# Kernel tuning notes

Measured on AMD Instinct MI355X. Metric: run time of the kernel, lower is better.

## Reference

```python
import jax, jax.numpy as jnp
from jax import lax
import numpy as np

B, INP, WIDTH, OUTP, E, H = 32, 1024, 256, 1024, 8, 14
EPS = 1e-5


def setup_inputs() -> dict:
    key = jax.random.key(0)
    ks = jax.random.split(key, 12)
    n = lambda k, s, sc=0.05: jax.random.normal(k, s, jnp.float32) * sc
    return {
        "x": jax.random.normal(ks[0], (B, INP, H, H), jnp.float32),
        "w1": n(ks[1], (E, WIDTH, INP, 1, 1)),
        "w2": n(ks[2], (E, WIDTH, WIDTH, 3, 3)),
        "w3": n(ks[3], (E, OUTP, WIDTH, 1, 1)),
        "r1_w": n(ks[4], (INP, E)), "r1_b": jnp.zeros((E,), jnp.float32),
        "r2_w": n(ks[5], (WIDTH, E)), "r2_b": jnp.zeros((E,), jnp.float32),
        "r3_w": n(ks[6], (WIDTH, E)), "r3_b": jnp.zeros((E,), jnp.float32),
        "bn1_g": jax.random.uniform(ks[7], (WIDTH,), jnp.float32, 0.5, 1.5),
        "bn1_b": n(ks[8], (WIDTH,), 0.1),
        "bn1_m": jnp.zeros((WIDTH,), jnp.float32), "bn1_v": jnp.ones((WIDTH,), jnp.float32),
        "bn2_g": jax.random.uniform(ks[9], (WIDTH,), jnp.float32, 0.5, 1.5),
        "bn2_b": n(ks[10], (WIDTH,), 0.1),
        "bn2_m": jnp.zeros((WIDTH,), jnp.float32), "bn2_v": jnp.ones((WIDTH,), jnp.float32),
        "bn3_g": jax.random.uniform(ks[11], (OUTP,), jnp.float32, 0.5, 1.5),
        "bn3_b": jnp.zeros((OUTP,), jnp.float32),
        "bn3_m": jnp.zeros((OUTP,), jnp.float32), "bn3_v": jnp.ones((OUTP,), jnp.float32),
    }


def _route(x, w, b):
    # global avg pool -> linear -> sigmoid : [B, E]
    return jax.nn.sigmoid(x.mean(axis=(2, 3)) @ w + b)


def _cond_conv(x, w, rw, stride=1, padding=0, dilation=1, groups=1):
    # x: [B,Cin,H,W]; w: [E,Cout,Cin/groups,kh,kw]; rw: [B,E]
    Bn, Cin, Hh, Ww = x.shape
    _, Cout, Cin_g, kh, kw = w.shape
    # per-sample expert-combined kernels, then batch-grouped conv
    cw = jnp.einsum('be,eoikl->boikl', rw, w).reshape(Bn * Cout, Cin_g, kh, kw)
    out = lax.conv_general_dilated(
        x.reshape(1, Bn * Cin, Hh, Ww), cw,
        window_strides=(stride, stride),
        padding=[(padding, padding), (padding, padding)],
        rhs_dilation=(dilation, dilation),
        feature_group_count=Bn * groups,
        dimension_numbers=('NCHW', 'OIHW', 'NCHW'))
    return out.reshape(Bn, Cout, out.shape[2], out.shape[3])


def _bn(x, g, b, m, v):
    inv = lax.rsqrt(v + EPS) * g
    return x * inv[None, :, None, None] + (b - m * inv)[None, :, None, None]


def reference(x, w1, w2, w3, r1_w, r1_b, r2_w, r2_b, r3_w, r3_b,
              bn1_g, bn1_b, bn1_m, bn1_v, bn2_g, bn2_b, bn2_m, bn2_v,
              bn3_g, bn3_b, bn3_m, bn3_v):
    identity = x
    rw1 = _route(x, r1_w, r1_b)
    out = jax.nn.relu(_bn(_cond_conv(x, w1, rw1), bn1_g, bn1_b, bn1_m, bn1_v))
    rw2 = _route(out, r2_w, r2_b)
    out = jax.nn.relu(_bn(_cond_conv(out, w2, rw2, stride=1, padding=1), bn2_g, bn2_b, bn2_m, bn2_v))
    rw3 = _route(out, r3_w, r3_b)
    out = _bn(_cond_conv(out, w3, rw3), bn3_g, bn3_b, bn3_m, bn3_v)
    return jax.nn.relu(out + identity)
```

## Files before the change

### kernel.cpp

```cpp
#include <hip/hip_runtime.h>
#include <hip/hip_bf16.h>

#define BB 32
#define INP 1024
#define WIDTH 256
#define OUTP 1024
#define NE 8
#define HW 196
#define HH 14
#define EPS 1e-5f

#define S1 (WIDTH * INP)
#define S2 (WIDTH * WIDTH * 9)
#define S3 (OUTP * WIDTH)

typedef __attribute__((ext_vector_type(8))) short bf16x8;
typedef __attribute__((ext_vector_type(4))) float f32x4;
typedef __attribute__((ext_vector_type(8))) unsigned short u16x8;


#define VMCNT(n) asm volatile("s_waitcnt vmcnt(" #n ")" ::: "memory")

__device__ __forceinline__ unsigned short f2bf_bits(float f) {
    unsigned u = __float_as_uint(f);
    u += 0x7FFFu + ((u >> 16) & 1u);
    return (unsigned short)(u >> 16);
}
__device__ __forceinline__ float bf2f(unsigned short h) {
    return __uint_as_float((unsigned)h << 16);
}

#if defined(__has_builtin)
#if __has_builtin(__builtin_amdgcn_global_load_lds)
#define HAVE_GLL 1
#endif
#endif
__device__ __forceinline__ void gl2lds(const unsigned short* g, unsigned short* l,
                                       int lane) {
#ifdef HAVE_GLL
    __builtin_amdgcn_global_load_lds(
        (const __attribute__((address_space(1))) unsigned int*)(const void*)g,
        (__attribute__((address_space(3))) unsigned int*)(void*)l, 16, 0, 0);
#else
    *(u16x8*)(l + lane * 8) = *(const u16x8*)g;
#endif
}

__device__ __forceinline__ void block_route(
    const float* __restrict__ vec, const float* __restrict__ W,
    const float* __restrict__ bias, float scale, int C, int g,
    float* srw, int tid) {
    int wv = tid >> 6, lane = tid & 63;
    float p0[NE], p1[NE];
#pragma unroll
    for (int e = 0; e < NE; e++) { p0[e] = 0.f; p1[e] = 0.f; }
    const float* v0 = vec + (size_t)(g * 8 + wv * 2) * C;
    const float* v1 = v0 + C;
    for (int c = lane; c < C; c += 64) {
        float4 wa = *(const float4*)(W + c * 8);
        float4 wb = *(const float4*)(W + c * 8 + 4);
        float m0 = v0[c], m1 = v1[c];
        p0[0] += m0 * wa.x; p0[1] += m0 * wa.y; p0[2] += m0 * wa.z; p0[3] += m0 * wa.w;
        p0[4] += m0 * wb.x; p0[5] += m0 * wb.y; p0[6] += m0 * wb.z; p0[7] += m0 * wb.w;
        p1[0] += m1 * wa.x; p1[1] += m1 * wa.y; p1[2] += m1 * wa.z; p1[3] += m1 * wa.w;
        p1[4] += m1 * wb.x; p1[5] += m1 * wb.y; p1[6] += m1 * wb.z; p1[7] += m1 * wb.w;
    }
#pragma unroll
    for (int j = 1; j < 64; j <<= 1) {
#pragma unroll
        for (int e = 0; e < NE; e++) {
            p0[e] += __shfl_xor(p0[e], j, 64);
            p1[e] += __shfl_xor(p1[e], j, 64);
        }
    }
    if (lane == 0) {
#pragma unroll
        for (int e = 0; e < NE; e++) {
            srw[(wv * 2) * 8 + e] = 1.0f / (1.0f + expf(-(scale * p0[e] + bias[e])));
            srw[(wv * 2 + 1) * 8 + e] = 1.0f / (1.0f + expf(-(scale * p1[e] + bias[e])));
        }
    }
    __syncthreads();
}

__global__ __launch_bounds__(256) void pre_kernel(
    const float* __restrict__ x, unsigned short* __restrict__ xb,
    float* __restrict__ mean1,
    const float* __restrict__ w2, unsigned short* __restrict__ wb2,
    unsigned short* __restrict__ zpad,
    float* __restrict__ msum2, float* __restrict__ msum3) {
    __shared__ __align__(16) char smem[128 * 17 * 4];
    int blk = blockIdx.x, t = threadIdx.x;
    if (blk < 256) {
        float (*lt)[17] = (float(*)[17])smem;
        int b = blk >> 3, yq = blk & 7, c0 = yq * 128;
        int cr = t >> 1, half = t & 1;
        const float* src = x + ((size_t)(b * INP + c0 + cr)) * HW;
        float msum = 0.f;
        int j = t >> 4, nl = t & 15;
        for (int pg = 0; pg < 14; pg++) {
            int p0 = pg * 16 + half * 8;
            float vv[8];
            if (pg < 12) {
                float4 a = *(const float4*)(src + p0);
                float4 c = *(const float4*)(src + p0 + 4);
                vv[0] = a.x; vv[1] = a.y; vv[2] = a.z; vv[3] = a.w;
                vv[4] = c.x; vv[5] = c.y; vv[6] = c.z; vv[7] = c.w;
            } else {
#pragma unroll
                for (int i = 0; i < 8; i++) {
                    int p = p0 + i;
                    vv[i] = (p < HW) ? src[p] : 0.f;
                }
            }
#pragma unroll
            for (int i = 0; i < 8; i++) { msum += vv[i]; lt[cr][half * 8 + i] = vv[i]; }
            __syncthreads();
            unsigned short pk[8];
#pragma unroll
            for (int i = 0; i < 8; i++) pk[i] = f2bf_bits(lt[j * 8 + i][nl]);
            size_t tile = ((size_t)b * 14 + pg) * 32 + (size_t)(yq * 4 + (j >> 2));
            int lane = nl | ((j & 3) << 4);
            *(u16x8*)(xb + tile * 512 + lane * 8) = *(u16x8*)pk;
            __syncthreads();
        }
        float other = __shfl_xor(msum, 1, 64);
        if (half == 0) mean1[b * INP + c0 + cr] = (msum + other) * (1.0f / (float)HW);
    } else {
        unsigned short* lds = (unsigned short*)smem;
        int eo = blk - 256;
        if (eo < 32) {
            int idx = eo * 256 + t;
            msum2[idx] = 0.f;
            msum3[idx] = 0.f;
            if (eo == 0 && t == 0) {
                u16x8 z = {0, 0, 0, 0, 0, 0, 0, 0};
                *(u16x8*)zpad = z;
            }
        }
        const float* src = w2 + (size_t)eo * 2304 + (size_t)t * 9;
#pragma unroll
        for (int t9 = 0; t9 < 9; t9++) lds[t9 * 256 + t] = f2bf_bits(src[t9]);
        __syncthreads();
        unsigned short* dst = wb2 + (size_t)eo * 2304;
        for (int j = t; j < 288; j += 256)
            *(u16x8*)(dst + j * 8) = *(const u16x8*)(lds + j * 8);
    }
}

__global__ __launch_bounds__(256) void combine_cont_r(
    const float* __restrict__ w, const float* __restrict__ vec,
    const float* __restrict__ rW, const float* __restrict__ rB, float scale, int C,
    unsigned short* __restrict__ cw, int S, int Mt, int Kt) {
    __shared__ float srw[64];
    int tid = threadIdx.x, wv = tid >> 6, lane = tid & 63, ml = lane & 15, k8l = lane >> 4;
    int g = blockIdx.y;
    block_route(vec, rW, rB, scale, C, g, srw, tid);
    int kq = Kt >> 2;
    int mt = blockIdx.x / kq, kt = (blockIdx.x - mt * kq) * 4 + wv;
    int K = Kt * 32;
    const float* src = w + (size_t)(mt * 16 + ml) * K + kt * 32 + k8l * 8;
    float v[NE][8];
#pragma unroll
    for (int e = 0; e < NE; e++) {
        float4 a = *(const float4*)(src + (size_t)e * S);
        float4 c = *(const float4*)(src + (size_t)e * S + 4);
        v[e][0] = a.x; v[e][1] = a.y; v[e][2] = a.z; v[e][3] = a.w;
        v[e][4] = c.x; v[e][5] = c.y; v[e][6] = c.z; v[e][7] = c.w;
    }
    size_t dto = ((size_t)mt * Kt + kt) * 512 + (size_t)lane * 8;
    size_t bstr = (size_t)Mt * Kt * 512;
    for (int bl = 0; bl < 8; bl++) {
        int b = g * 8 + bl;
        float acc[8];
#pragma unroll
        for (int jj = 0; jj < 8; jj++) acc[jj] = 0.f;
#pragma unroll
        for (int e = 0; e < NE; e++) {
            float r = srw[bl * NE + e];
#pragma unroll
            for (int jj = 0; jj < 8; jj++) acc[jj] += r * v[e][jj];
        }
        u16x8 o;
#pragma unroll
        for (int jj = 0; jj < 8; jj++) o[jj] = f2bf_bits(acc[jj]);
        *(u16x8*)(cw + (size_t)b * bstr + dto) = o;
    }
}

__global__ __launch_bounds__(256) void combine_w2_r(
    const unsigned short* __restrict__ wb2, const float* __restrict__ vec,
    const float* __restrict__ rW, const float* __restrict__ rB, float scale,
    unsigned short* __restrict__ cw) {
    __shared__ float srw[64];
    int tid = threadIdx.x, wv = tid >> 6, lane = tid & 63, ol = lane & 15, g4 = lane >> 4;
    int g = blockIdx.y;
    block_route(vec, rW, rB, scale, 256, g, srw, tid);
    int ot = blockIdx.x / 18, kt = (blockIdx.x - ot * 18) * 4 + wv;
    const unsigned short* src = wb2 + (size_t)(ot * 16 + ol) * 2304 + kt * 32 + g4 * 8;
    float v[NE][8];
#pragma unroll
    for (int e = 0; e < NE; e++) {
        u16x8 raw = *(const u16x8*)(src + (size_t)e * S2);
#pragma unroll
        for (int jj = 0; jj < 8; jj++) v[e][jj] = bf2f(raw[jj]);
    }
    size_t dto = ((size_t)ot * 72 + kt) * 512 + (size_t)lane * 8;
    for (int bl = 0; bl < 8; bl++) {
        int b = g * 8 + bl;
        float acc[8];
#pragma unroll
        for (int jj = 0; jj < 8; jj++) acc[jj] = 0.f;
#pragma unroll
        for (int e = 0; e < NE; e++) {
            float r = srw[bl * NE + e];
#pragma unroll
            for (int jj = 0; jj < 8; jj++) acc[jj] += r * v[e][jj];
        }
        u16x8 out;
#pragma unroll
        for (int jj = 0; jj < 8; jj++) out[jj] = f2bf_bits(acc[jj]);
        *(u16x8*)(cw + (size_t)b * (16 * 72 * 512) + dto) = out;
    }
}

__device__ __forceinline__ void epilogue_act(
    const f32x4* acc, int b, int mt, int nt0, int nB, int lo, int g4,
    const float* __restrict__ g, const float* __restrict__ be,
    const float* __restrict__ mu, const float* __restrict__ var,
    unsigned short* __restrict__ actout, float* __restrict__ msum) {
    int c0 = mt * 16 + g4 * 4;
    float sc[4], sh[4];
#pragma unroll
    for (int r = 0; r < 4; r++) {
        float iv = rsqrtf(var[c0 + r] + EPS) * g[c0 + r];
        sc[r] = iv;
        sh[r] = be[c0 + r] - mu[c0 + r] * iv;
    }
    float ms[4] = {0.f, 0.f, 0.f, 0.f};
    int ktc = mt >> 1;
    int lanehi = ((mt * 2 + (g4 >> 1)) & 3) << 4;
#pragma unroll
    for (int t = 0; t < 4; t++) {
        if (t >= nB) break;
        int nt = nt0 + t;
        int n = nt * 16 + lo;
        float v[4];
#pragma unroll
        for (int r = 0; r < 4; r++) {
            float val = acc[t][r] * sc[r] + sh[r];
            val = fmaxf(val, 0.f);
            if (n >= HW) val = 0.f;
            v[r] = val;
            ms[r] += val;
        }
        unsigned p01 = (unsigned)f2bf_bits(v[0]) | ((unsigned)f2bf_bits(v[1]) << 16);
        unsigned p23 = (unsigned)f2bf_bits(v[2]) | ((unsigned)f2bf_bits(v[3]) << 16);
        size_t off = (((size_t)(b * 14 + nt)) * 8 + ktc) * 512 + (size_t)(lo | lanehi) * 8 + (g4 & 1) * 4;
        *(uint2*)(actout + off) = make_uint2(p01, p23);
    }
#pragma unroll
    for (int r = 0; r < 4; r++) {
        float s = ms[r];
        s += __shfl_xor(s, 1, 64);
        s += __shfl_xor(s, 2, 64);
        s += __shfl_xor(s, 4, 64);
        s += __shfl_xor(s, 8, 64);
        if (lo == 0) atomicAdd(&msum[b * 256 + c0 + r], s);
    }
}

__global__ __launch_bounds__(512) void gemm1_fused(
    const unsigned short* __restrict__ Bsw, const unsigned short* __restrict__ Asw,
    const float* __restrict__ g, const float* __restrict__ be,
    const float* __restrict__ mu, const float* __restrict__ var,
    unsigned short* __restrict__ actout, float* __restrict__ msum) {
    __shared__ __align__(16) unsigned short lAb[8][4 * 512];
    __shared__ __align__(16) unsigned short lBb[8][4 * 512];
    const int Kt = 32;
    int b = blockIdx.x, mh = blockIdx.y, z = blockIdx.z;
    int nt0 = (z < 3) ? z * 4 : 11;
    int nB = (z < 2) ? 4 : 3;
    int tid = threadIdx.x, wv = tid >> 6, grp = wv >> 2, wl = wv & 3;
    int lane = tid & 63, lo = lane & 15, g4 = lane >> 4;
    const unsigned short* Ab = Asw + (size_t)(b * 16 + mh * 4) * Kt * 512;
    const unsigned short* Bb = Bsw + (size_t)(b * 14 + nt0) * Kt * 512;
    f32x4 acc[4];
#pragma unroll
    for (int t = 0; t < 4; t++) acc[t] = {0.f, 0.f, 0.f, 0.f};

    auto stage = [&](int kt) {
        unsigned short* lA = lAb[kt & 7];
        unsigned short* lB = lBb[kt & 7];
        gl2lds(Ab + ((size_t)wl * Kt + kt) * 512 + lane * 8, lA + wl * 512, lane);
        if (wl < nB)
            gl2lds(Bb + ((size_t)wl * Kt + kt) * 512 + lane * 8, lB + wl * 512, lane);
    };
    auto compute = [&](int kt) {
        const unsigned short* lA = lAb[kt & 7];
        const unsigned short* lB = lBb[kt & 7];
        bf16x8 a0 = *(const bf16x8*)(lA + wl * 512 + lane * 8);
#pragma unroll
        for (int t = 0; t < 4; t++) {
            if (t >= nB) break;
            bf16x8 bt = *(const bf16x8*)(lB + t * 512 + lane * 8);
            acc[t] = __builtin_amdgcn_mfma_f32_16x16x32_bf16(a0, bt, acc[t], 0, 0, 0);
        }
    };

    stage(grp);
    stage(grp + 2);
    for (int kp = 0; kp < 16; kp++) {
        int c = 2 * kp + grp;
        if (c + 2 < 32) {
            if (wl < nB) VMCNT(2); else VMCNT(1);
        } else {
            VMCNT(0);
        }
        __builtin_amdgcn_s_barrier();
        int s = c + 4;
        if (s < 32) stage(s);
        compute(c);
    }
    __syncthreads();
    float* red = (float*)&lBb[0][0];
    if (grp == 1) {
#pragma unroll
        for (int t = 0; t < 4; t++)
            *(f32x4*)(red + (((size_t)wl * 4 + t) * 64 + lane) * 4) = acc[t];
    }
    __syncthreads();
    if (grp == 0) {
#pragma unroll
        for (int t = 0; t < 4; t++) {
            f32x4 o = *(const f32x4*)(red + (((size_t)wl * 4 + t) * 64 + lane) * 4);
#pragma unroll
            for (int r = 0; r < 4; r++) acc[t][r] += o[r];
        }
        epilogue_act(acc, b, mh * 4 + wl, nt0, nB, lo, g4, g, be, mu, var, actout, msum);
    }
}

__global__ __launch_bounds__(512) void gemm2_fused(
    const unsigned short* __restrict__ act, const unsigned short* __restrict__ cw2,
    const unsigned short* __restrict__ zpad,
    const float* __restrict__ g, const float* __restrict__ be,
    const float* __restrict__ mu, const float* __restrict__ var,
    unsigned short* __restrict__ actout, float* __restrict__ msum) {
    __shared__ __align__(16) unsigned short lAb[8][4 * 512];
    __shared__ __align__(16) unsigned short lBb[8][4 * 512];
    int b = blockIdx.x, mh = blockIdx.y, z = blockIdx.z;
    int nt0 = (z < 3) ? z * 4 : 11;
    int nB = (z < 2) ? 4 : 3;
    int tid = threadIdx.x, wv = tid >> 6, grp = wv >> 2, wl = wv & 3;
    int lane = tid & 63, lo = lane & 15, g4 = lane >> 4;
    const unsigned short* Ab = cw2 + (size_t)(b * 16 + mh * 4) * 72 * 512;
    const unsigned short* actb = act + (size_t)b * 14 * 8 * 512;

    int p0 = (nt0 + wl) * 16 + lo;
    int py0 = p0 / HH, px0 = p0 - (p0 / HH) * HH;
    bool pv0 = (wl < nB) && (p0 < HW);

    f32x4 acc[4];
#pragma unroll
    for (int t = 0; t < 4; t++) acc[t] = {0.f, 0.f, 0.f, 0.f};

    auto stage = [&](int kt) {
        unsigned short* lA = lAb[kt & 7];
        unsigned short* lB = lBb[kt & 7];
        gl2lds(Ab + ((size_t)wl * 72 + kt) * 512 + lane * 8, lA + wl * 512, lane);
        if (wl < nB) {
            int t9 = kt >> 3;
            int dy = t9 / 3 - 1, dx = t9 - (t9 / 3) * 3 - 1;
            int itile = kt & 7;
            int sy = py0 + dy, sx = px0 + dx;
            bool ok = pv0 && sy >= 0 && sy < HH && sx >= 0 && sx < HH;
            int ns = sy * HH + sx;
            const unsigned short* gp = ok
                ? actb + ((size_t)(ns >> 4) * 8 + itile) * 512 + (size_t)((ns & 15) | (g4 << 4)) * 8
                : zpad;
            gl2lds(gp, lB + wl * 512, lane);
        }
    };
    auto compute = [&](int kt) {
        const unsigned short* lA = lAb[kt & 7];
        const unsigned short* lB = lBb[kt & 7];
        bf16x8 a0 = *(const bf16x8*)(lA + wl * 512 + lane * 8);
#pragma unroll
        for (int t = 0; t < 4; t++) {
            if (t >= nB) break;
            bf16x8 bt = *(const bf16x8*)(lB + t * 512 + lane * 8);
            acc[t] = __builtin_amdgcn_mfma_f32_16x16x32_bf16(a0, bt, acc[t], 0, 0, 0);
        }
    };

    stage(grp);
    stage(grp + 2);
    for (int kp = 0; kp < 36; kp++) {
        int c = 2 * kp + grp;
        if (c + 2 < 72) {
            if (wl < nB) VMCNT(2); else VMCNT(1);
        } else {
            VMCNT(0);
        }
        __builtin_amdgcn_s_barrier();
        int s = c + 4;
        if (s < 72) stage(s);
        compute(c);
    }
    __syncthreads();
    float* red = (float*)&lBb[0][0];
    if (grp == 1) {
#pragma unroll
        for (int t = 0; t < 4; t++)
            *(f32x4*)(red + (((size_t)wl * 4 + t) * 64 + lane) * 4) = acc[t];
    }
    __syncthreads();
    if (grp == 0) {
#pragma unroll
        for (int t = 0; t < 4; t++) {
            f32x4 o = *(const f32x4*)(red + (((size_t)wl * 4 + t) * 64 + lane) * 4);
#pragma unroll
            for (int r = 0; r < 4; r++) acc[t][r] += o[r];
        }
        epilogue_act(acc, b, mh * 4 + wl, nt0, nB, lo, g4, g, be, mu, var, actout, msum);
    }
}

__global__ __launch_bounds__(512) void gemm3_fused(
    const unsigned short* __restrict__ Bsw, const unsigned short* __restrict__ Asw,
    const float* __restrict__ g, const float* __restrict__ be,
    const float* __restrict__ mu, const float* __restrict__ var,
    const unsigned short* __restrict__ xb, float* __restrict__ out) {
    __shared__ __align__(16) unsigned short lAb[4][8 * 512];
    __shared__ __align__(16) unsigned short lBb[4][7 * 512];
    int b = blockIdx.x, y = blockIdx.y, mh = y >> 1, nh = y & 1;
    int tid = threadIdx.x, wv = tid >> 6, grp = wv >> 2, wl = wv & 3;
    int lane = tid & 63, lo = lane & 15, g4 = lane >> 4;
    const unsigned short* Ab = Asw + (size_t)(b * 64 + mh * 8) * 8 * 512;
    const unsigned short* Bb = Bsw + (size_t)(b * 14 + nh * 7) * 8 * 512;
    f32x4 acc0[7], acc1[7];
#pragma unroll
    for (int t = 0; t < 7; t++) { acc0[t] = {0.f, 0.f, 0.f, 0.f}; acc1[t] = {0.f, 0.f, 0.f, 0.f}; }

    auto stage = [&](int kt, unsigned short* lA, unsigned short* lB) {
        gl2lds(Ab + ((size_t)wl * 8 + kt) * 512 + lane * 8, lA + wl * 512, lane);
        gl2lds(Ab + ((size_t)(wl + 4) * 8 + kt) * 512 + lane * 8, lA + (wl + 4) * 512, lane);
        gl2lds(Bb + ((size_t)wl * 8 + kt) * 512 + lane * 8, lB + wl * 512, lane);
        if (wl < 3)
            gl2lds(Bb + ((size_t)(4 + wl) * 8 + kt) * 512 + lane * 8, lB + (4 + wl) * 512, lane);
    };
    auto compute = [&](const unsigned short* lA, const unsigned short* lB) {
        bf16x8 a0 = *(const bf16x8*)(lA + wl * 512 + lane * 8);
        bf16x8 a1 = *(const bf16x8*)(lA + (wl + 4) * 512 + lane * 8);
#pragma unroll
        for (int t = 0; t < 7; t++) {
            bf16x8 bt = *(const bf16x8*)(lB + t * 512 + lane * 8);
            acc0[t] = __builtin_amdgcn_mfma_f32_16x16x32_bf16(a0, bt, acc0[t], 0, 0, 0);
            acc1[t] = __builtin_amdgcn_mfma_f32_16x16x32_bf16(a1, bt, acc1[t], 0, 0, 0);
        }
    };

    stage(grp, lAb[grp], lBb[grp]);
    for (int kp = 0; kp < 4; kp++) {
        __syncthreads();
        if (kp < 3) {
            int s = 2 * kp + 2 + grp;
            stage(s, lAb[s & 3], lBb[s & 3]);
        }
        int c = (2 * kp + grp) & 3;
        compute(lAb[c], lBb[c]);
    }
    __syncthreads();
    float* red = (float*)&lBb[0][0];
    if (grp == 1) {
#pragma unroll
        for (int t = 0; t < 7; t++)
            *(f32x4*)(red + (((size_t)wl * 7 + t) * 64 + lane) * 4) = acc0[t];
    }
    __syncthreads();
    if (grp == 0) {
#pragma unroll
        for (int t = 0; t < 7; t++) {
            f32x4 o = *(const f32x4*)(red + (((size_t)wl * 7 + t) * 64 + lane) * 4);
#pragma unroll
            for (int r = 0; r < 4; r++) acc0[t][r] += o[r];
        }
    }
    __syncthreads();
    if (grp == 1) {
#pragma unroll
        for (int t = 0; t < 7; t++)
            *(f32x4*)(red + (((size_t)wl * 7 + t) * 64 + lane) * 4) = acc1[t];
    }
    __syncthreads();
    if (grp != 0) return;
#pragma unroll
    for (int t = 0; t < 7; t++) {
        f32x4 o = *(const f32x4*)(red + (((size_t)wl * 7 + t) * 64 + lane) * 4);
#pragma unroll
        for (int r = 0; r < 4; r++) acc1[t][r] += o[r];
    }

#pragma unroll
    for (int a = 0; a < 2; a++) {
        int mt = mh * 8 + wl + 4 * a;
        int c0 = mt * 16 + g4 * 4;
        float sc[4], sh[4];
#pragma unroll
        for (int r = 0; r < 4; r++) {
            float iv = rsqrtf(var[c0 + r] + EPS) * g[c0 + r];
            sc[r] = iv;
            sh[r] = be[c0 + r] - mu[c0 + r] * iv;
        }
        int ktc = mt >> 1;
        int lanehi = ((mt * 2 + (g4 >> 1)) & 3) << 4;
#pragma unroll
        for (int t = 0; t < 7; t++) {
            int nt = nh * 7 + t;
            int n = nt * 16 + lo;
            if (n >= HW) continue;
            const unsigned short* xr = xb + (((size_t)(b * 14 + nt)) * 32 + ktc) * 512
                                       + (size_t)(lo | lanehi) * 8 + (g4 & 1) * 4;
            uint2 rv = *(const uint2*)xr;
            float res[4] = {bf2f((unsigned short)(rv.x & 0xffff)),
                            bf2f((unsigned short)(rv.x >> 16)),
                            bf2f((unsigned short)(rv.y & 0xffff)),
                            bf2f((unsigned short)(rv.y >> 16))};
            f32x4 av = a ? acc1[t] : acc0[t];
#pragma unroll
            for (int r = 0; r < 4; r++) {
                size_t oidx = ((size_t)(b * OUTP + c0 + r)) * HW + n;
                float val = av[r] * sc[r] + sh[r] + res[r];
                out[oidx] = fmaxf(val, 0.f);
            }
        }
    }
}

extern "C" void kernel_launch(void* const* d_in, const int* in_sizes, int n_in,
                              void* d_out, int out_size, void* d_ws, size_t ws_size,
                              hipStream_t stream) {
    const float* x    = (const float*)d_in[0];
    const float* w1   = (const float*)d_in[1];
    const float* w2   = (const float*)d_in[2];
    const float* w3   = (const float*)d_in[3];
    const float* r1_w = (const float*)d_in[4];
    const float* r1_b = (const float*)d_in[5];
    const float* r2_w = (const float*)d_in[6];
    const float* r2_b = (const float*)d_in[7];
    const float* r3_w = (const float*)d_in[8];
    const float* r3_b = (const float*)d_in[9];
    const float* bn1_g = (const float*)d_in[10];
    const float* bn1_b = (const float*)d_in[11];
    const float* bn1_m = (const float*)d_in[12];
    const float* bn1_v = (const float*)d_in[13];
    const float* bn2_g = (const float*)d_in[14];
    const float* bn2_b = (const float*)d_in[15];
    const float* bn2_m = (const float*)d_in[16];
    const float* bn2_v = (const float*)d_in[17];
    const float* bn3_g = (const float*)d_in[18];
    const float* bn3_b = (const float*)d_in[19];
    const float* bn3_m = (const float*)d_in[20];
    const float* bn3_v = (const float*)d_in[21];
    float* out = (float*)d_out;

    char* ws = (char*)d_ws;
    size_t off = 0;
    float* mean1 = (float*)(ws + off); off += (size_t)BB * INP * 4;
    float* msum2 = (float*)(ws + off); off += (size_t)BB * 256 * 4;
    float* msum3 = (float*)(ws + off); off += (size_t)BB * 256 * 4;
    unsigned short* zpad = (unsigned short*)(ws + off); off += 256;
    off = (off + 255) & ~(size_t)255;
    unsigned short* act1 = (unsigned short*)(ws + off); off += (size_t)BB * 14 * 8 * 512 * 2;
    unsigned short* act2 = (unsigned short*)(ws + off); off += (size_t)BB * 14 * 8 * 512 * 2;
    unsigned short* cw2 = (unsigned short*)(ws + off); off += (size_t)BB * 16 * 72 * 512 * 2;
    unsigned short* xb  = (unsigned short*)(ws + off); off += (size_t)BB * 14 * 32 * 512 * 2;
    unsigned short* wb2 = (unsigned short*)(ws + off); off += (size_t)S2 * NE * 2;
    unsigned short* cwX = (unsigned short*)(ws + off); off += (size_t)BB * S1 * 2;
    unsigned short* cw1 = cwX;
    unsigned short* cw3 = cwX;
    (void)ws_size;

    pre_kernel<<<2304, 256, 0, stream>>>(x, xb, mean1, w2, wb2, zpad, msum2, msum3);

    combine_cont_r<<<dim3(128, 4), 256, 0, stream>>>(w1, mean1, r1_w, r1_b, 1.0f, INP,
                                                     cw1, S1, 16, 32);
    gemm1_fused<<<dim3(BB, 4, 4), 512, 0, stream>>>(xb, cw1, bn1_g, bn1_b, bn1_m, bn1_v,
                                                    act1, msum2);

    combine_w2_r<<<dim3(288, 4), 256, 0, stream>>>(wb2, msum2, r2_w, r2_b,
                                                   1.0f / (float)HW, cw2);
    gemm2_fused<<<dim3(BB, 4, 4), 512, 0, stream>>>(act1, cw2, zpad, bn2_g, bn2_b,
                                                    bn2_m, bn2_v, act2, msum3);

    combine_cont_r<<<dim3(128, 4), 256, 0, stream>>>(w3, msum3, r3_w, r3_b,
                                                     1.0f / (float)HW, WIDTH,
                                                     cw3, S3, 64, 8);
    gemm3_fused<<<dim3(BB, 16), 512, 0, stream>>>(act2, cw3, bn3_g, bn3_b, bn3_m, bn3_v,
                                                  xb, out);
}
```

Before: 243.3 us.

## Fuse all seven stages into one cooperative persistent kernel with grid syncs

Replaces the chain of seven kernel launches with a single cooperative mega-kernel of 512 blocks that runs each phase (pre-pack, combines, three GEMMs) separated by grid.sync barriers. This removes launch overhead and inter-kernel gaps. Phases that used more blocks (e.g. pre_kernel with 2304 blocks) are remapped onto 512 blocks. The old multi-kernel path remains as a fallback when the stream is being captured or occupancy is insufficient. The cost is grid-wide barriers, 64KB static LDS per block limiting occupancy, and phases with lower parallelism per block.

```diff
diff --git a/kernel.cpp b/kernel.cpp
--- a/kernel.cpp
+++ b/kernel.cpp
@@ -1,5 +1,8 @@
 #include <hip/hip_runtime.h>
 #include <hip/hip_bf16.h>
+#include <hip/hip_cooperative_groups.h>
+
+namespace cg = cooperative_groups;
 
 #define BB 32
 #define INP 1024
@@ -45,6 +48,7 @@
     *(u16x8*)(l + lane * 8) = *(const u16x8*)g;
 #endif
 }
+
 
 __device__ __forceinline__ void block_route(
     const float* __restrict__ vec, const float* __restrict__ W,
@@ -538,65 +542,566 @@
     }
 }
 
+
+struct MegaP {
+    const float *x, *w1, *w2, *w3;
+    const float *r1w, *r1b, *r2w, *r2b, *r3w, *r3b;
+    const float *bn1g, *bn1b, *bn1m, *bn1v;
+    const float *bn2g, *bn2b, *bn2m, *bn2v;
+    const float *bn3g, *bn3b, *bn3m, *bn3v;
+    float* out;
+    float *mean1, *msum2, *msum3;
+    unsigned short *zpad, *act1, *act2, *cw2, *xb, *wb2, *cwX;
+};
+
+__device__ __forceinline__ void route512(
+    const float* vec, const float* W, const float* bias, float scale, int C,
+    int g, float* srw, int tid) {
+    int wv = tid >> 6, lane = tid & 63;
+    float pp[NE];
+#pragma unroll
+    for (int e = 0; e < NE; e++) pp[e] = 0.f;
+    const float* v0 = vec + (size_t)(g * 8 + wv) * C;
+    for (int c = lane; c < C; c += 64) {
+        float4 wa = *(const float4*)(W + c * 8);
+        float4 wb = *(const float4*)(W + c * 8 + 4);
+        float m = v0[c];
+        pp[0] += m * wa.x; pp[1] += m * wa.y; pp[2] += m * wa.z; pp[3] += m * wa.w;
+        pp[4] += m * wb.x; pp[5] += m * wb.y; pp[6] += m * wb.z; pp[7] += m * wb.w;
+    }
+#pragma unroll
+    for (int j = 1; j < 64; j <<= 1) {
+#pragma unroll
+        for (int e = 0; e < NE; e++) pp[e] += __shfl_xor(pp[e], j, 64);
+    }
+    if (lane == 0) {
+#pragma unroll
+        for (int e = 0; e < NE; e++)
+            srw[wv * 8 + e] = 1.0f / (1.0f + expf(-(scale * pp[e] + bias[e])));
+    }
+    __syncthreads();
+}
+
+__device__ __forceinline__ void phase_pre(const MegaP& p, char* smem, int r, int tid) {
+    if (r < 256) {
+        float (*lt)[17] = (float(*)[17])smem;
+        bool act = tid < 256;
+        int b = r >> 3, yq = r & 7, c0 = yq * 128;
+        int cr = tid >> 1, half = tid & 1;
+        const float* src = act ? p.x + ((size_t)(b * INP + c0 + cr)) * HW : p.x;
+        float msum = 0.f;
+        int j = tid >> 4, nl = tid & 15;
+        for (int pg = 0; pg < 14; pg++) {
+            if (act) {
+                int p0 = pg * 16 + half * 8;
+                float vv[8];
+                if (pg < 12) {
+                    float4 a = *(const float4*)(src + p0);
+                    float4 c = *(const float4*)(src + p0 + 4);
+                    vv[0] = a.x; vv[1] = a.y; vv[2] = a.z; vv[3] = a.w;
+                    vv[4] = c.x; vv[5] = c.y; vv[6] = c.z; vv[7] = c.w;
+                } else {
+#pragma unroll
+                    for (int i = 0; i < 8; i++) {
+                        int pp = p0 + i;
+                        vv[i] = (pp < HW) ? src[pp] : 0.f;
+                    }
+                }
+#pragma unroll
+                for (int i = 0; i < 8; i++) { msum += vv[i]; lt[cr][half * 8 + i] = vv[i]; }
+            }
+            __syncthreads();
+            if (act) {
+                unsigned short pk[8];
+#pragma unroll
+                for (int i = 0; i < 8; i++) pk[i] = f2bf_bits(lt[j * 8 + i][nl]);
+                size_t tile = ((size_t)b * 14 + pg) * 32 + (size_t)(yq * 4 + (j >> 2));
+                int lane = nl | ((j & 3) << 4);
+                *(u16x8*)(p.xb + tile * 512 + lane * 8) = *(u16x8*)pk;
+            }
+            __syncthreads();
+        }
+        if (act) {
+            float other = __shfl_xor(msum, 1, 64);
+            if (half == 0) p.mean1[b * INP + c0 + cr] = (msum + other) * (1.0f / (float)HW);
+        }
+    } else {
+        int rb = r - 256;
+        int sub = tid >> 8, vt = tid & 255;
+        unsigned short* lds = (unsigned short*)smem + sub * 2304;
+        if (rb < 32 && tid < 256) {
+            int idx = rb * 256 + tid;
+            p.msum2[idx] = 0.f;
+            p.msum3[idx] = 0.f;
+        }
+        if (rb == 0 && tid == 0) {
+            u16x8 z = {0, 0, 0, 0, 0, 0, 0, 0};
+            *(u16x8*)p.zpad = z;
+        }
+        for (int it = 0; it < 4; it++) {
+            int eo = rb * 8 + it * 2 + sub;
+            const float* s2 = p.w2 + (size_t)eo * 2304 + (size_t)vt * 9;
+#pragma unroll
+            for (int t9 = 0; t9 < 9; t9++) lds[t9 * 256 + vt] = f2bf_bits(s2[t9]);
+            __syncthreads();
+            unsigned short* dst = p.wb2 + (size_t)eo * 2304;
+            for (int jj = vt; jj < 288; jj += 256)
+                *(u16x8*)(dst + jj * 8) = *(const u16x8*)(lds + jj * 8);
+            __syncthreads();
+        }
+    }
+}
+
+__device__ __forceinline__ void phase_combine_cont(
+    const float* w, const float* vec, const float* rW, const float* rB,
+    float scale, int C, unsigned short* cw, int S, int Mt, int Kt,
+    char* smem, int r, int tid) {
+    if (r >= 256) return;
+    float* srw = (float*)smem;
+    int wv = tid >> 6, lane = tid & 63, ml = lane & 15, k8l = lane >> 4;
+    int g = r & 3, xp = r >> 2;
+    route512(vec, rW, rB, scale, C, g, srw, tid);
+    int kq8 = Kt >> 3;
+    int mt = xp / kq8, kt = (xp - mt * kq8) * 8 + wv;
+    int K = Kt * 32;
+    const float* src = w + (size_t)(mt * 16 + ml) * K + kt * 32 + k8l * 8;
+    float v[NE][8];
+#pragma unroll
+    for (int e = 0; e < NE; e++) {
+        float4 a = *(const float4*)(src + (size_t)e * S);
+        float4 c = *(const float4*)(src + (size_t)e * S + 4);
+        v[e][0] = a.x; v[e][1] = a.y; v[e][2] = a.z; v[e][3] = a.w;
+        v[e][4] = c.x; v[e][5] = c.y; v[e][6] = c.z; v[e][7] = c.w;
+    }
+    size_t dto = ((size_t)mt * Kt + kt) * 512 + (size_t)lane * 8;
+    size_t bstr = (size_t)Mt * Kt * 512;
+    for (int bl = 0; bl < 8; bl++) {
+        int b = g * 8 + bl;
+        float acc[8];
+#pragma unroll
+        for (int jj = 0; jj < 8; jj++) acc[jj] = 0.f;
+#pragma unroll
+        for (int e = 0; e < NE; e++) {
+            float rr = srw[bl * NE + e];
+#pragma unroll
+            for (int jj = 0; jj < 8; jj++) acc[jj] += rr * v[e][jj];
+        }
+        u16x8 o;
+#pragma unroll
+        for (int jj = 0; jj < 8; jj++) o[jj] = f2bf_bits(acc[jj]);
+        *(u16x8*)(cw + (size_t)b * bstr + dto) = o;
+    }
+}
+
+__device__ __forceinline__ void phase_combine_w2(const MegaP& p, char* smem,
+                                                 int r, int tid) {
+    float* srw = (float*)smem;
+    int wv = tid >> 6, lane = tid & 63, ol = lane & 15, g4 = lane >> 4;
+    int g = r & 3, u = r >> 2;
+    route512(p.msum2, p.r2w, p.r2b, 1.0f / (float)HW, 256, g, srw, tid);
+    for (int it = 0; it < 2; it++) {
+        int bx;
+        if (it == 0) bx = u + (wv >= 4 ? 128 : 0);
+        else {
+            if (wv >= 4 || u >= 32) break;
+            bx = u + 256;
+        }
+        int ot = bx / 18, ktq = bx - ot * 18;
+        int kt = ktq * 4 + (wv & 3);
+        const unsigned short* src = p.wb2 + (size_t)(ot * 16 + ol) * 2304 + kt * 32 + g4 * 8;
+        float v[NE][8];
+#pragma unroll
+        for (int e = 0; e < NE; e++) {
+            u16x8 raw = *(const u16x8*)(src + (size_t)e * S2);
+#pragma unroll
+            for (int jj = 0; jj < 8; jj++) v[e][jj] = bf2f(raw[jj]);
+        }
+        size_t dto = ((size_t)ot * 72 + kt) * 512 + (size_t)lane * 8;
+        for (int bl = 0; bl < 8; bl++) {
+            int b = g * 8 + bl;
+            float acc[8];
+#pragma unroll
+            for (int jj = 0; jj < 8; jj++) acc[jj] = 0.f;
+#pragma unroll
+            for (int e = 0; e < NE; e++) {
+                float rr = srw[bl * NE + e];
+#pragma unroll
+                for (int jj = 0; jj < 8; jj++) acc[jj] += rr * v[e][jj];
+            }
+            u16x8 o;
+#pragma unroll
+            for (int jj = 0; jj < 8; jj++) o[jj] = f2bf_bits(acc[jj]);
+            *(u16x8*)(p.cw2 + (size_t)b * (16 * 72 * 512) + dto) = o;
+        }
+    }
+}
+
+__device__ __forceinline__ void phase_gemm1(const MegaP& p, char* smem, int r, int tid) {
+    unsigned short (*lAb)[4 * 512] = (unsigned short(*)[4 * 512])smem;
+    unsigned short (*lBb)[4 * 512] = (unsigned short(*)[4 * 512])(smem + 32768);
+    const int Kt = 32;
+    int b = r >> 4, mh = (r >> 2) & 3, z = r & 3;
+    int nt0 = (z < 3) ? z * 4 : 11;
+    int nB = (z < 2) ? 4 : 3;
+    int wv = tid >> 6, grp = wv >> 2, wl = wv & 3;
+    int lane = tid & 63, lo = lane & 15, g4 = lane >> 4;
+    const unsigned short* Ab = p.cwX + (size_t)(b * 16 + mh * 4) * Kt * 512;
+    const unsigned short* Bb = p.xb + (size_t)(b * 14 + nt0) * Kt * 512;
+    f32x4 acc[4];
+#pragma unroll
+    for (int t = 0; t < 4; t++) acc[t] = {0.f, 0.f, 0.f, 0.f};
+
+    auto stage = [&](int kt) {
+        unsigned short* lA = lAb[kt & 7];
+        unsigned short* lB = lBb[kt & 7];
+        gl2lds(Ab + ((size_t)wl * Kt + kt) * 512 + lane * 8, lA + wl * 512, lane);
+        if (wl < nB)
+            gl2lds(Bb + ((size_t)wl * Kt + kt) * 512 + lane * 8, lB + wl * 512, lane);
+    };
+    auto compute = [&](int kt) {
+        const unsigned short* lA = lAb[kt & 7];
+        const unsigned short* lB = lBb[kt & 7];
+        bf16x8 a0 = *(const bf16x8*)(lA + wl * 512 + lane * 8);
+#pragma unroll
+        for (int t = 0; t < 4; t++) {
+            if (t >= nB) break;
+            bf16x8 bt = *(const bf16x8*)(lB + t * 512 + lane * 8);
+            acc[t] = __builtin_amdgcn_mfma_f32_16x16x32_bf16(a0, bt, acc[t], 0, 0, 0);
+        }
+    };
+
+    stage(grp);
+    stage(grp + 2);
+    for (int kp = 0; kp < 16; kp++) {
+        int c = 2 * kp + grp;
+        if (c + 2 < 32) {
+            if (wl < nB) VMCNT(2); else VMCNT(1);
+        } else {
+            VMCNT(0);
+        }
+        __builtin_amdgcn_s_barrier();
+        int s = c + 4;
+        if (s < 32) stage(s);
+        compute(c);
+    }
+    __syncthreads();
+    float* red = (float*)&lBb[0][0];
+    if (grp == 1) {
+#pragma unroll
+        for (int t = 0; t < 4; t++)
+            *(f32x4*)(red + (((size_t)wl * 4 + t) * 64 + lane) * 4) = acc[t];
+    }
+    __syncthreads();
+    if (grp == 0) {
+#pragma unroll
+        for (int t = 0; t < 4; t++) {
+            f32x4 o = *(const f32x4*)(red + (((size_t)wl * 4 + t) * 64 + lane) * 4);
+#pragma unroll
+            for (int rr = 0; rr < 4; rr++) acc[t][rr] += o[rr];
+        }
+        epilogue_act(acc, b, mh * 4 + wl, nt0, nB, lo, g4,
+                     p.bn1g, p.bn1b, p.bn1m, p.bn1v, p.act1, p.msum2);
+    }
+}
+
+__device__ __forceinline__ void phase_gemm2(const MegaP& p, char* smem, int r, int tid) {
+    unsigned short (*lAb)[4 * 512] = (unsigned short(*)[4 * 512])smem;
+    unsigned short (*lBb)[4 * 512] = (unsigned short(*)[4 * 512])(smem + 32768);
+    int b = r >> 4, mh = (r >> 2) & 3, z = r & 3;
+    int nt0 = (z < 3) ? z * 4 : 11;
+    int nB = (z < 2) ? 4 : 3;
+    int wv = tid >> 6, grp = wv >> 2, wl = wv & 3;
+    int lane = tid & 63, lo = lane & 15, g4 = lane >> 4;
+    const unsigned short* Ab = p.cw2 + (size_t)(b * 16 + mh * 4) * 72 * 512;
+    const unsigned short* actb = p.act1 + (size_t)b * 14 * 8 * 512;
+
+    int p0 = (nt0 + wl) * 16 + lo;
+    int py0 = p0 / HH, px0 = p0 - (p0 / HH) * HH;
+    bool pv0 = (wl < nB) && (p0 < HW);
+
+    f32x4 acc[4];
+#pragma unroll
+    for (int t = 0; t < 4; t++) acc[t] = {0.f, 0.f, 0.f, 0.f};
+
+    auto stage = [&](int kt) {
+        unsigned short* lA = lAb[kt & 7];
+        unsigned short* lB = lBb[kt & 7];
+        gl2lds(Ab + ((size_t)wl * 72 + kt) * 512 + lane * 8, lA + wl * 512, lane);
+        if (wl < nB) {
+            int t9 = kt >> 3;
+            int dy = t9 / 3 - 1, dx = t9 - (t9 / 3) * 3 - 1;
+            int itile = kt & 7;
+            int sy = py0 + dy, sx = px0 + dx;
+            bool ok = pv0 && sy >= 0 && sy < HH && sx >= 0 && sx < HH;
+            int ns = sy * HH + sx;
+            const unsigned short* gp = ok
+                ? actb + ((size_t)(ns >> 4) * 8 + itile) * 512 + (size_t)((ns & 15) | (g4 << 4)) * 8
+                : p.zpad;
+            gl2lds(gp, lB + wl * 512, lane);
+        }
+    };
+    auto compute = [&](int kt) {
+        const unsigned short* lA = lAb[kt & 7];
+        const unsigned short* lB = lBb[kt & 7];
+        bf16x8 a0 = *(const bf16x8*)(lA + wl * 512 + lane * 8);
+#pragma unroll
+        for (int t = 0; t < 4; t++) {
+            if (t >= nB) break;
+            bf16x8 bt = *(const bf16x8*)(lB + t * 512 + lane * 8);
+            acc[t] = __builtin_amdgcn_mfma_f32_16x16x32_bf16(a0, bt, acc[t], 0, 0, 0);
+        }
+    };
+
+    stage(grp);
+    stage(grp + 2);
+    for (int kp = 0; kp < 36; kp++) {
+        int c = 2 * kp + grp;
+        if (c + 2 < 72) {
+            if (wl < nB) VMCNT(2); else VMCNT(1);
+        } else {
+            VMCNT(0);
+        }
+        __builtin_amdgcn_s_barrier();
+        int s = c + 4;
+        if (s < 72) stage(s);
+        compute(c);
+    }
+    __syncthreads();
+    float* red = (float*)&lBb[0][0];
+    if (grp == 1) {
+#pragma unroll
+        for (int t = 0; t < 4; t++)
+            *(f32x4*)(red + (((size_t)wl * 4 + t) * 64 + lane) * 4) = acc[t];
+    }
+    __syncthreads();
+    if (grp == 0) {
+#pragma unroll
+        for (int t = 0; t < 4; t++) {
+            f32x4 o = *(const f32x4*)(red + (((size_t)wl * 4 + t) * 64 + lane) * 4);
+#pragma unroll
+            for (int rr = 0; rr < 4; rr++) acc[t][rr] += o[rr];
+        }
+        epilogue_act(acc, b, mh * 4 + wl, nt0, nB, lo, g4,
+                     p.bn2g, p.bn2b, p.bn2m, p.bn2v, p.act2, p.msum3);
+    }
+}
+
+__device__ __forceinline__ void phase_gemm3(const MegaP& p, char* smem, int r, int tid) {
+    unsigned short (*lAb)[8 * 512] = (unsigned short(*)[8 * 512])smem;
+    unsigned short (*lBb)[7 * 512] = (unsigned short(*)[7 * 512])(smem + 32768);
+    int b = r >> 4, y = r & 15, mh = y >> 1, nh = y & 1;
+    int wv = tid >> 6, grp = wv >> 2, wl = wv & 3;
+    int lane = tid & 63, lo = lane & 15, g4 = lane >> 4;
+    const unsigned short* Ab = p.cwX + (size_t)(b * 64 + mh * 8) * 8 * 512;
+    const unsigned short* Bb = p.act2 + (size_t)(b * 14 + nh * 7) * 8 * 512;
+    f32x4 acc0[7], acc1[7];
+#pragma unroll
+    for (int t = 0; t < 7; t++) { acc0[t] = {0.f, 0.f, 0.f, 0.f}; acc1[t] = {0.f, 0.f, 0.f, 0.f}; }
+
+    auto stage = [&](int kt, unsigned short* lA, unsigned short* lB) {
+        gl2lds(Ab + ((size_t)wl * 8 + kt) * 512 + lane * 8, lA + wl * 512, lane);
+        gl2lds(Ab + ((size_t)(wl + 4) * 8 + kt) * 512 + lane * 8, lA + (wl + 4) * 512, lane);
+        gl2lds(Bb + ((size_t)wl * 8 + kt) * 512 + lane * 8, lB + wl * 512, lane);
+        if (wl < 3)
+            gl2lds(Bb + ((size_t)(4 + wl) * 8 + kt) * 512 + lane * 8, lB + (4 + wl) * 512, lane);
+    };
+    auto compute = [&](const unsigned short* lA, const unsigned short* lB) {
+        bf16x8 a0 = *(const bf16x8*)(lA + wl * 512 + lane * 8);
+        bf16x8 a1 = *(const bf16x8*)(lA + (wl + 4) * 512 + lane * 8);
+#pragma unroll
+        for (int t = 0; t < 7; t++) {
+            bf16x8 bt = *(const bf16x8*)(lB + t * 512 + lane * 8);
+            acc0[t] = __builtin_amdgcn_mfma_f32_16x16x32_bf16(a0, bt, acc0[t], 0, 0, 0);
+            acc1[t] = __builtin_amdgcn_mfma_f32_16x16x32_bf16(a1, bt, acc1[t], 0, 0, 0);
+        }
+    };
+
+    stage(grp, lAb[grp], lBb[grp]);
+    for (int kp = 0; kp < 4; kp++) {
+        __syncthreads();
+        if (kp < 3) {
+            int s = 2 * kp + 2 + grp;
+            stage(s, lAb[s & 3], lBb[s & 3]);
+        }
+        int c = (2 * kp + grp) & 3;
+        compute(lAb[c], lBb[c]);
+    }
+    __syncthreads();
+    float* red = (float*)&lBb[0][0];
+    if (grp == 1) {
+#pragma unroll
+        for (int t = 0; t < 7; t++)
+            *(f32x4*)(red + (((size_t)wl * 7 + t) * 64 + lane) * 4) = acc0[t];
+    }
+    __syncthreads();
+    if (grp == 0) {
+#pragma unroll
+        for (int t = 0; t < 7; t++) {
+            f32x4 o = *(const f32x4*)(red + (((size_t)wl * 7 + t) * 64 + lane) * 4);
+#pragma unroll
+            for (int rr = 0; rr < 4; rr++) acc0[t][rr] += o[rr];
+        }
+    }
+    __syncthreads();
+    if (grp == 1) {
+#pragma unroll
+        for (int t = 0; t < 7; t++)
+            *(f32x4*)(red + (((size_t)wl * 7 + t) * 64 + lane) * 4) = acc1[t];
+    }
+    __syncthreads();
+    if (grp != 0) return;
+#pragma unroll
+    for (int t = 0; t < 7; t++) {
+        f32x4 o = *(const f32x4*)(red + (((size_t)wl * 7 + t) * 64 + lane) * 4);
+#pragma unroll
+        for (int rr = 0; rr < 4; rr++) acc1[t][rr] += o[rr];
+    }
+
+#pragma unroll
+    for (int a = 0; a < 2; a++) {
+        int mt = mh * 8 + wl + 4 * a;
+        int c0 = mt * 16 + g4 * 4;
+        float sc[4], sh[4];
+#pragma unroll
+        for (int rr = 0; rr < 4; rr++) {
+            float iv = rsqrtf(p.bn3v[c0 + rr] + EPS) * p.bn3g[c0 + rr];
+            sc[rr] = iv;
+            sh[rr] = p.bn3b[c0 + rr] - p.bn3m[c0 + rr] * iv;
+        }
+        int ktc = mt >> 1;
+        int lanehi = ((mt * 2 + (g4 >> 1)) & 3) << 4;
+#pragma unroll
+        for (int t = 0; t < 7; t++) {
+            int nt = nh * 7 + t;
+            int n = nt * 16 + lo;
+            if (n >= HW) continue;
+            const unsigned short* xr = p.xb + (((size_t)(b * 14 + nt)) * 32 + ktc) * 512
+                                       + (size_t)(lo | lanehi) * 8 + (g4 & 1) * 4;
+            uint2 rv = *(const uint2*)xr;
+            float res[4] = {bf2f((unsigned short)(rv.x & 0xffff)),
+                            bf2f((unsigned short)(rv.x >> 16)),
+                            bf2f((unsigned short)(rv.y & 0xffff)),
+                            bf2f((unsigned short)(rv.y >> 16))};
+            f32x4 av = a ? acc1[t] : acc0[t];
+#pragma unroll
+            for (int rr = 0; rr < 4; rr++) {
+                size_t oidx = ((size_t)(b * OUTP + c0 + rr)) * HW + n;
+                float val = av[rr] * sc[rr] + sh[rr] + res[rr];
+                p.out[oidx] = fmaxf(val, 0.f);
+            }
+        }
+    }
+}
+
+__global__ __launch_bounds__(512, 4) void mega_kernel(MegaP p) {
+    __shared__ __align__(16) char smem[65536];
+    cg::grid_group grid = cg::this_grid();
+    const int r = blockIdx.x;
+    const int tid = threadIdx.x;
+
+    phase_pre(p, smem, r, tid);
+    __threadfence(); grid.sync(); __threadfence();
+
+    phase_combine_cont(p.w1, p.mean1, p.r1w, p.r1b, 1.0f, INP,
+                       p.cwX, S1, 16, 32, smem, r, tid);
+    __threadfence(); grid.sync(); __threadfence();
+
+    phase_gemm1(p, smem, r, tid);
+    __threadfence(); grid.sync(); __threadfence();
+
+    phase_combine_w2(p, smem, r, tid);
+    __threadfence(); grid.sync(); __threadfence();
+
+    phase_gemm2(p, smem, r, tid);
+    __threadfence(); grid.sync(); __threadfence();
+
+    phase_combine_cont(p.w3, p.msum3, p.r3w, p.r3b, 1.0f / (float)HW, WIDTH,
+                       p.cwX, S3, 64, 8, smem, r, tid);
+    __threadfence(); grid.sync(); __threadfence();
+
+    phase_gemm3(p, smem, r, tid);
+}
+
 extern "C" void kernel_launch(void* const* d_in, const int* in_sizes, int n_in,
                               void* d_out, int out_size, void* d_ws, size_t ws_size,
                               hipStream_t stream) {
-    const float* x    = (const float*)d_in[0];
-    const float* w1   = (const float*)d_in[1];
-    const float* w2   = (const float*)d_in[2];
-    const float* w3   = (const float*)d_in[3];
-    const float* r1_w = (const float*)d_in[4];
-    const float* r1_b = (const float*)d_in[5];
-    const float* r2_w = (const float*)d_in[6];
-    const float* r2_b = (const float*)d_in[7];
-    const float* r3_w = (const float*)d_in[8];
-    const float* r3_b = (const float*)d_in[9];
-    const float* bn1_g = (const float*)d_in[10];
-    const float* bn1_b = (const float*)d_in[11];
-    const float* bn1_m = (const float*)d_in[12];
-    const float* bn1_v = (const float*)d_in[13];
-    const float* bn2_g = (const float*)d_in[14];
-    const float* bn2_b = (const float*)d_in[15];
-    const float* bn2_m = (const float*)d_in[16];
-    const float* bn2_v = (const float*)d_in[17];
-    const float* bn3_g = (const float*)d_in[18];
-    const float* bn3_b = (const float*)d_in[19];
-    const float* bn3_m = (const float*)d_in[20];
-    const float* bn3_v = (const float*)d_in[21];
-    float* out = (float*)d_out;
+    (void)in_sizes; (void)n_in; (void)out_size; (void)ws_size;
+    MegaP p;
+    p.x    = (const float*)d_in[0];
+    p.w1   = (const float*)d_in[1];
+    p.w2   = (const float*)d_in[2];
+    p.w3   = (const float*)d_in[3];
+    p.r1w  = (const float*)d_in[4];
+    p.r1b  = (const float*)d_in[5];
+    p.r2w  = (const float*)d_in[6];
+    p.r2b  = (const float*)d_in[7];
+    p.r3w  = (const float*)d_in[8];
+    p.r3b  = (const float*)d_in[9];
+    p.bn1g = (const float*)d_in[10];
+    p.bn1b = (const float*)d_in[11];
+    p.bn1m = (const float*)d_in[12];
+    p.bn1v = (const float*)d_in[13];
+    p.bn2g = (const float*)d_in[14];
+    p.bn2b = (const float*)d_in[15];
+    p.bn2m = (const float*)d_in[16];
+    p.bn2v = (const float*)d_in[17];
+    p.bn3g = (const float*)d_in[18];
+    p.bn3b = (const float*)d_in[19];
+    p.bn3m = (const float*)d_in[20];
+    p.bn3v = (const float*)d_in[21];
+    p.out  = (float*)d_out;
 
     char* ws = (char*)d_ws;
     size_t off = 0;
-    float* mean1 = (float*)(ws + off); off += (size_t)BB * INP * 4;
-    float* msum2 = (float*)(ws + off); off += (size_t)BB * 256 * 4;
-    float* msum3 = (float*)(ws + off); off += (size_t)BB * 256 * 4;
-    unsigned short* zpad = (unsigned short*)(ws + off); off += 256;
+    p.mean1 = (float*)(ws + off); off += (size_t)BB * INP * 4;
+    p.msum2 = (float*)(ws + off); off += (size_t)BB * 256 * 4;
+    p.msum3 = (float*)(ws + off); off += (size_t)BB * 256 * 4;
+    p.zpad  = (unsigned short*)(ws + off); off += 256;
     off = (off + 255) & ~(size_t)255;
-    unsigned short* act1 = (unsigned short*)(ws + off); off += (size_t)BB * 14 * 8 * 512 * 2;
-    unsigned short* act2 = (unsigned short*)(ws + off); off += (size_t)BB * 14 * 8 * 512 * 2;
-    unsigned short* cw2 = (unsigned short*)(ws + off); off += (size_t)BB * 16 * 72 * 512 * 2;
-    unsigned short* xb  = (unsigned short*)(ws + off); off += (size_t)BB * 14 * 32 * 512 * 2;
-    unsigned short* wb2 = (unsigned short*)(ws + off); off += (size_t)S2 * NE * 2;
-    unsigned short* cwX = (unsigned short*)(ws + off); off += (size_t)BB * S1 * 2;
-    unsigned short* cw1 = cwX;
-    unsigned short* cw3 = cwX;
-    (void)ws_size;
-
-    pre_kernel<<<2304, 256, 0, stream>>>(x, xb, mean1, w2, wb2, zpad, msum2, msum3);
-
-    combine_cont_r<<<dim3(128, 4), 256, 0, stream>>>(w1, mean1, r1_w, r1_b, 1.0f, INP,
-                                                     cw1, S1, 16, 32);
-    gemm1_fused<<<dim3(BB, 4, 4), 512, 0, stream>>>(xb, cw1, bn1_g, bn1_b, bn1_m, bn1_v,
-                                                    act1, msum2);
-
-    combine_w2_r<<<dim3(288, 4), 256, 0, stream>>>(wb2, msum2, r2_w, r2_b,
-                                                   1.0f / (float)HW, cw2);
-    gemm2_fused<<<dim3(BB, 4, 4), 512, 0, stream>>>(act1, cw2, zpad, bn2_g, bn2_b,
-                                                    bn2_m, bn2_v, act2, msum3);
-
-    combine_cont_r<<<dim3(128, 4), 256, 0, stream>>>(w3, msum3, r3_w, r3_b,
+    p.act1 = (unsigned short*)(ws + off); off += (size_t)BB * 14 * 8 * 512 * 2;
+    p.act2 = (unsigned short*)(ws + off); off += (size_t)BB * 14 * 8 * 512 * 2;
+    p.cw2  = (unsigned short*)(ws + off); off += (size_t)BB * 16 * 72 * 512 * 2;
+    p.xb   = (unsigned short*)(ws + off); off += (size_t)BB * 14 * 32 * 512 * 2;
+    p.wb2  = (unsigned short*)(ws + off); off += (size_t)S2 * NE * 2;
+    p.cwX  = (unsigned short*)(ws + off); off += (size_t)BB * S1 * 2;
+
+    bool use_coop = false;
+    hipStreamCaptureStatus cst = hipStreamCaptureStatusNone;
+    if (hipStreamIsCapturing(stream, &cst) == hipSuccess &&
+        cst == hipStreamCaptureStatusNone) {
+        int maxb = 0;
+        if (hipOccupancyMaxActiveBlocksPerMultiprocessor(
+                &maxb, (const void*)mega_kernel, 512, 0) == hipSuccess) {
+            int dev = 0, ncu = 0;
+            hipGetDevice(&dev);
+            hipDeviceGetAttribute(&ncu, hipDeviceAttributeMultiprocessorCount, dev);
+            if (maxb > 0 && (long long)maxb * ncu >= 512) use_coop = true;
+        }
+    }
+    if (use_coop) {
+        void* args[] = {(void*)&p};
+        if (hipLaunchCooperativeKernel((void*)mega_kernel, dim3(512), dim3(512),
+                                       args, 0, stream) == hipSuccess)
+            return;
+    }
+
+    pre_kernel<<<2304, 256, 0, stream>>>(p.x, p.xb, p.mean1, p.w2, p.wb2,
+                                         p.zpad, p.msum2, p.msum3);
+
+    combine_cont_r<<<dim3(128, 4), 256, 0, stream>>>(p.w1, p.mean1, p.r1w, p.r1b,
+                                                     1.0f, INP, p.cwX, S1, 16, 32);
+    gemm1_fused<<<dim3(BB, 4, 4), 512, 0, stream>>>(p.xb, p.cwX, p.bn1g, p.bn1b,
+                                                    p.bn1m, p.bn1v, p.act1, p.msum2);
+
+    combine_w2_r<<<dim3(288, 4), 256, 0, stream>>>(p.wb2, p.msum2, p.r2w, p.r2b,
+                                                   1.0f / (float)HW, p.cw2);
+    gemm2_fused<<<dim3(BB, 4, 4), 512, 0, stream>>>(p.act1, p.cw2, p.zpad, p.bn2g,
+                                                    p.bn2b, p.bn2m, p.bn2v, p.act2,
+                                                    p.msum3);
+
+    combine_cont_r<<<dim3(128, 4), 256, 0, stream>>>(p.w3, p.msum3, p.r3w, p.r3b,
                                                      1.0f / (float)HW, WIDTH,
-                                                     cw3, S3, 64, 8);
-    gemm3_fused<<<dim3(BB, 16), 512, 0, stream>>>(act2, cw3, bn3_g, bn3_b, bn3_m, bn3_v,
-                                                  xb, out);
-}
+                                                     p.cwX, S3, 64, 8);
+    gemm3_fused<<<dim3(BB, 16), 512, 0, stream>>>(p.act2, p.cwX, p.bn3g, p.bn3b,
+                                                  p.bn3m, p.bn3v, p.xb, p.out);
+}
```

Measured after the change: 239.0 us. About the same (-1.8%).
